# Kernel optimization log

Hardware: AMD Instinct MI355X
Metric: run time of the kernel (lower is better)

Reference implementation:

```python
import jax, jax.numpy as jnp
import numpy as np

TOP_K = 8
ALPHA = 0.1
EPS = 1e-20


def setup_inputs() -> dict:
    key = jax.random.key(0)
    k1, k2 = jax.random.split(key)
    B, S, D, E = 4, 8192, 1024, 64
    hidden_states = jax.random.normal(k1, (B, S, D), dtype=jnp.float32)
    # kaiming_uniform_(a=sqrt(5)) on [E, D] -> bound = 1/sqrt(D)
    bound = 1.0 / np.sqrt(D)
    W = jax.random.uniform(k2, (E, D), dtype=jnp.float32, minval=-bound, maxval=bound)
    return {"hidden_states": hidden_states, "W": W}


def reference(hidden_states, W):
    B, S, D = hidden_states.shape
    E = W.shape[0]
    x = hidden_states.reshape(-1, D)                       # [T, D], T = B*S
    logits = jnp.einsum('td,ed->te', x, W)                 # [T, E]
    scores = jax.nn.softmax(logits, axis=-1)               # [T, E]
    top_k_weights, top_k_idx = jax.lax.top_k(scores, TOP_K)  # [T, K]
    # norm_topk_experts renormalization
    top_k_weights = top_k_weights / (top_k_weights.sum(axis=-1, keepdims=True) + EPS)
    # seq_aux loss: per-batch expert selection counts via scatter-add
    idx = top_k_idx.reshape(B, -1)                         # [B, S*K]
    ce = jnp.zeros((B, E), dtype=jnp.float32).at[jnp.arange(B)[:, None], idx].add(1.0)
    mean_scores = scores.reshape(B, S, E).mean(axis=1)     # [B, E]
    aux_loss = (ce * mean_scores).sum(axis=1).mean() * ALPHA
    return top_k_idx, top_k_weights, aux_loss
```

## Files before the change

### kernel.cpp

```cpp
#include <hip/hip_runtime.h>

#define TOKS   32768
#define NEXP   64
#define DDIM   1024
#define SEQ    8192
#define NBATCH 4
#define TPB    64
#define STR    68
#define CSTR   21
#define BK     64
#define NCHK   (DDIM / BK)
#define WTILE  16384
#define XTILE  16384

typedef __attribute__((ext_vector_type(8)))  short short8v;
typedef __attribute__((ext_vector_type(16))) float f32x16;

__device__ __forceinline__ unsigned f2bf(float x) {
  unsigned u = __float_as_uint(x);
  return (u + 0x7fffu + ((u >> 16) & 1u)) >> 16;
}
__device__ __forceinline__ float bf2f(unsigned h) { return __uint_as_float(h << 16); }

__device__ __forceinline__ void gload_lds16(const void* g, void* s) {
  __builtin_amdgcn_global_load_lds(
      (const __attribute__((address_space(1))) unsigned int*)g,
      (__attribute__((address_space(3))) unsigned int*)s, 16, 0, 0);
}

__device__ __forceinline__ void conv8(const float4 p0, const float4 p1,
                                      unsigned* h, unsigned* lo) {
  float ff[8] = {p0.x, p0.y, p0.z, p0.w, p1.x, p1.y, p1.z, p1.w};
#pragma unroll
  for (int i = 0; i < 4; ++i) {
    unsigned h0 = f2bf(ff[2 * i]), h1 = f2bf(ff[2 * i + 1]);
    h[i] = h0 | (h1 << 16);
    unsigned l0 = f2bf(ff[2 * i] - bf2f(h0));
    unsigned l1 = f2bf(ff[2 * i + 1] - bf2f(h1));
    lo[i] = l0 | (l1 << 16);
  }
}

__global__ void moe_wsplit(const float* __restrict__ W, ushort* __restrict__ W2) {
  const int sid = blockIdx.x * 256 + threadIdx.x;
  const int p  = sid & 15;
  const int e  = (sid >> 4) & 63;
  const int kc = sid >> 10;
  const int sl = p ^ (e & 15);
  const int k0 = kc * BK + (sl & 7) * 8;
  const float* src = W + (size_t)e * DDIM + k0;
  float f[8];
  *(float4*)&f[0] = *(const float4*)src;
  *(float4*)&f[4] = *(const float4*)(src + 4);
  ushort o[8];
  if (sl < 8) {
#pragma unroll
    for (int j = 0; j < 8; ++j) o[j] = (ushort)f2bf(f[j]);
  } else {
#pragma unroll
    for (int j = 0; j < 8; ++j) {
      unsigned hb = f2bf(f[j]);
      o[j] = (ushort)f2bf(f[j] - bf2f(hb));
    }
  }
  *(short8v*)(W2 + (size_t)sid * 8) = *(const short8v*)o;
}

__global__ __launch_bounds__(256, 2) void moe_gate_main(
    const float* __restrict__ X, const ushort* __restrict__ W2,
    float* __restrict__ out, float* __restrict__ gsum, float* __restrict__ gce,
    int* __restrict__ flag_cnt, int* __restrict__ flag_tok)
{
  __shared__ __align__(16) char smem[65536];

  float* xs   = (float*)smem;
  float* wsm  = (float*)(smem + 17408);
  float* red  = (float*)(smem + 34816);
  float* gmx  = (float*)(smem + 35840);
  float* cval = (float*)(smem + 36096);
  int*   cidx = (int*)  (smem + 41472);
  int*   hist = (int*)  (smem + 46848);

  const int tid = threadIdx.x;
  const int tok_base = blockIdx.x * TPB;
  const int bb = blockIdx.x >> 7;

  const int l = tid & 63, q = tid >> 6;
  const int wm = q >> 1, wn = q & 1;
  const int rr = l & 31;
  const int kh = l >> 5;

  const char* Xb = (const char*)X + (size_t)tok_base * DDIM * 4;
  int gofs[4];
#pragma unroll
  for (int i = 0; i < 4; ++i) {
    const int r  = 16 * q + 4 * i + (l >> 4);
    const int sl = (l & 15) ^ (r & 15);
    gofs[i] = r * 4096 + sl * 16;
  }
  const char* w2c = (const char*)W2;

  const int arow = (wm * 32 + rr) * 256;
  const int brow = (wn * 32 + rr) * 256;
  const int rxor = rr & 15;

  f32x16 accA = (f32x16)0.0f, accB = (f32x16)0.0f;

#pragma unroll
  for (int i = 0; i < 4; ++i)
    gload_lds16(Xb + gofs[i], smem + q * 4096 + i * 1024);
#pragma unroll
  for (int i = 0; i < 4; ++i)
    gload_lds16(w2c + q * 4096 + i * 1024 + l * 16, smem + 32768 + q * 4096 + i * 1024);
  __syncthreads();

  int cur = 0;
#pragma unroll 1
  for (int kc = 0; kc < NCHK; ++kc) {
    if (kc + 1 < NCHK) {
      const char* xg = Xb + (kc + 1) * 256;
      char* xd = smem + (cur ^ 1) * XTILE + q * 4096;
#pragma unroll
      for (int i = 0; i < 4; ++i) gload_lds16(xg + gofs[i], xd + i * 1024);
      const char* wg = w2c + (size_t)(kc + 1) * WTILE + q * 4096 + l * 16;
      char* wd = smem + 32768 + (cur ^ 1) * WTILE + q * 4096;
#pragma unroll
      for (int i = 0; i < 4; ++i) gload_lds16(wg + i * 1024, wd + i * 1024);
    }
    const char* ta = smem + cur * XTILE + arow;
    const char* tb = smem + 32768 + cur * WTILE + brow;
#pragma unroll
    for (int s = 0; s < 4; ++s) {
      const int q0 = 4 * s + 2 * kh;
      float4 f0 = *(const float4*)(ta + ((q0 ^ rxor) * 16));
      float4 f1 = *(const float4*)(ta + (((q0 + 1) ^ rxor) * 16));
      unsigned ah[4], al[4];
      conv8(f0, f1, ah, al);
      short8v bh = *(const short8v*)(tb + (((2 * s + kh) ^ rxor) * 16));
      short8v bl = *(const short8v*)(tb + (((8 + 2 * s + kh) ^ rxor) * 16));
      union { short8v v; unsigned u[4]; } ua, ul;
#pragma unroll
      for (int i = 0; i < 4; ++i) { ua.u[i] = ah[i]; ul.u[i] = al[i]; }
      accA = __builtin_amdgcn_mfma_f32_32x32x16_bf16(ua.v, bh, accA, 0, 0, 0);
      accB = __builtin_amdgcn_mfma_f32_32x32x16_bf16(ul.v, bh, accB, 0, 0, 0);
      accA = __builtin_amdgcn_mfma_f32_32x32x16_bf16(ua.v, bl, accA, 0, 0, 0);
    }
    __syncthreads();
    cur ^= 1;
  }

  {
    const int ccol = wn * 32 + rr;
#pragma unroll
    for (int r = 0; r < 16; ++r) {
      const int trow = wm * 32 + (r & 3) + 8 * (r >> 2) + 4 * kh;
      wsm[trow * STR + ccol] = accA[r] + accB[r];
    }
  }
  if (tid < 64) hist[tid] = 0;
  __syncthreads();

  float* logits  = wsm;
  float* scoresT = xs;
  const int t = l;

  float m = -__builtin_huge_valf();
#pragma unroll
  for (int e = 0; e < 16; ++e) m = fmaxf(m, logits[t * STR + q * 16 + e]);
  red[q * 64 + t] = m;
  __syncthreads();
  float gm = fmaxf(fmaxf(red[t], red[64 + t]), fmaxf(red[128 + t], red[192 + t]));
  if (q == 0) gmx[t] = gm;
  float z = 0.0f;
#pragma unroll
  for (int e = 0; e < 16; ++e) {
    float ev = expf(logits[t * STR + q * 16 + e] - gm);
    scoresT[(q * 16 + e) * STR + t] = ev;
    z += ev;
  }
  __syncthreads();
  red[q * 64 + t] = z;
  __syncthreads();
  float Z = red[t] + red[64 + t] + red[128 + t] + red[192 + t];
  float invZ = 1.0f / Z;
#pragma unroll
  for (int e = 0; e < 16; ++e) scoresT[(q * 16 + e) * STR + t] *= invZ;
  __syncthreads();

  {
    const int e = l, g = q;
    float s = 0.0f;
#pragma unroll
    for (int tt = 0; tt < 16; ++tt) s += scoresT[e * STR + g * 16 + tt];
    red[g * 64 + e] = s;
  }
  __syncthreads();
  if (tid < 64) {
    float tot = red[tid] + red[64 + tid] + red[128 + tid] + red[192 + tid];
    atomicAdd(&gsum[bb * 64 + tid], tot);
  }

  if (tid < 128) {
    const int h = tid >> 6;
    const int eb = h * 32;
#pragma unroll 1
    for (int k = 0; k < 9; ++k) {
      float mv = -1.0f; int mi = eb;
#pragma unroll 4
      for (int e = 0; e < 32; ++e) {
        float v = scoresT[(eb + e) * STR + t];
        if (v > mv) { mv = v; mi = eb + e; }
      }
      cval[t * CSTR + h * 9 + k] = mv;
      cidx[t * CSTR + h * 9 + k] = mi;
      scoresT[mi * STR + t] = -1.0f;
    }
  }
  __syncthreads();

  if (tid < 64) {
    float wv[9]; int wi[8];
#pragma unroll 1
    for (int k = 0; k < 9; ++k) {
      float mv = -1.0f; int mj = 0;
#pragma unroll 3
      for (int j = 0; j < 18; ++j) {
        float v = cval[t * CSTR + j];
        if (v > mv) { mv = v; mj = j; }
      }
      wv[k] = mv;
      if (k < 8) {
        wi[k] = cidx[t * CSTR + mj];
        atomicAdd(&hist[wi[k]], 1);
      }
      cval[t * CSTR + mj] = -1.0f;
    }
    bool flag = false;
#pragma unroll
    for (int k = 0; k < 8; ++k)
      if (wv[k + 1] >= wv[k] * (1.0f - 2.0e-5f)) flag = true;
    if (flag) {
      int p = atomicAdd(flag_cnt, 1);
      flag_tok[p] = tok_base + t;
    }
    double ed[8]; double den = 0.0;
#pragma unroll
    for (int k = 0; k < 8; ++k) {
      ed[k] = exp((double)logits[t * STR + wi[k]] - (double)gmx[t]);
      den += ed[k];
    }
    const size_t tg = (size_t)(tok_base + t);
    *(float4*)(out + tg * 8) =
        make_float4((float)wi[0], (float)wi[1], (float)wi[2], (float)wi[3]);
    *(float4*)(out + tg * 8 + 4) =
        make_float4((float)wi[4], (float)wi[5], (float)wi[6], (float)wi[7]);
    *(float4*)(out + (size_t)TOKS * 8 + tg * 8) =
        make_float4((float)(ed[0] / den), (float)(ed[1] / den),
                    (float)(ed[2] / den), (float)(ed[3] / den));
    *(float4*)(out + (size_t)TOKS * 8 + tg * 8 + 4) =
        make_float4((float)(ed[4] / den), (float)(ed[5] / den),
                    (float)(ed[6] / den), (float)(ed[7] / den));
  }
  __syncthreads();
  if (tid < 64) atomicAdd(&gce[bb * 64 + tid], (float)hist[tid]);
}

__global__ __launch_bounds__(256) void moe_refine(
    const float* __restrict__ X, const float* __restrict__ W,
    float* __restrict__ out, float* __restrict__ gce,
    const int* __restrict__ flag_cnt, const int* __restrict__ flag_tok)
{
  __shared__ __align__(16) float xrow[DDIM];
  __shared__ double part[4][NEXP];
  const int tid = threadIdx.x;
  const int n = *flag_cnt;
  const int e = tid & 63;
  const int c = tid >> 6;
#pragma unroll 1
  for (int it = blockIdx.x; it < n; it += 256) {
    const int tok = flag_tok[it];
    __syncthreads();
    *(float4*)&xrow[tid * 4] = *(const float4*)&X[(size_t)tok * DDIM + tid * 4];
    __syncthreads();
    const float* wr = W + (size_t)e * DDIM + c * 256;
    const float* xr = xrow + c * 256;
    double s0 = 0.0, s1 = 0.0, s2 = 0.0, s3 = 0.0;
#pragma unroll 4
    for (int j = 0; j < 256; j += 4) {
      s0 += (double)xr[j]     * (double)wr[j];
      s1 += (double)xr[j + 1] * (double)wr[j + 1];
      s2 += (double)xr[j + 2] * (double)wr[j + 2];
      s3 += (double)xr[j + 3] * (double)wr[j + 3];
    }
    part[c][e] = (s0 + s1) + (s2 + s3);
    __syncthreads();
    if (tid < 64) {
      double cur = (part[0][e] + part[1][e]) + (part[2][e] + part[3][e]);
      int wi[8]; double wl[8];
#pragma unroll 1
      for (int k = 0; k < 8; ++k) {
        double mv = cur; int mi = e;
#pragma unroll
        for (int off = 1; off < 64; off <<= 1) {
          double ov = __shfl_xor(mv, off);
          int    oi = __shfl_xor(mi, off);
          if (ov > mv || (ov == mv && oi < mi)) { mv = ov; mi = oi; }
        }
        wi[k] = mi; wl[k] = mv;
        if (e == mi) cur = -1.0e300;
      }
      if (e == 0) {
        int olde[8];
#pragma unroll
        for (int k = 0; k < 8; ++k) olde[k] = (int)out[(size_t)tok * 8 + k];
        double ex[8]; double den = 0.0;
#pragma unroll
        for (int k = 0; k < 8; ++k) { ex[k] = exp(wl[k] - wl[0]); den += ex[k]; }
#pragma unroll
        for (int k = 0; k < 8; ++k) {
          out[(size_t)tok * 8 + k] = (float)wi[k];
          out[(size_t)TOKS * 8 + (size_t)tok * 8 + k] = (float)(ex[k] / den);
        }
        const int bbb = tok >> 13;
#pragma unroll 1
        for (int k = 0; k < 8; ++k) {
          bool in_new = false, in_old = false;
          for (int j = 0; j < 8; ++j) {
            if (wi[j] == olde[k]) in_new = true;
            if (olde[j] == wi[k]) in_old = true;
          }
          if (!in_new) atomicAdd(&gce[bbb * 64 + olde[k]], -1.0f);
          if (!in_old) atomicAdd(&gce[bbb * 64 + wi[k]], 1.0f);
        }
      }
    }
  }
}

__global__ void moe_gate_aux(const float* __restrict__ gsum,
                             const float* __restrict__ gce,
                             float* __restrict__ out)
{
  __shared__ float r[256];
  const int tid = threadIdx.x;
  r[tid] = gce[tid] * gsum[tid];
  __syncthreads();
  for (int s = 128; s > 0; s >>= 1) {
    if (tid < s) r[tid] += r[tid + s];
    __syncthreads();
  }
  if (tid == 0)
    out[(size_t)TOKS * 16] = 0.1f * r[0] / ((float)SEQ * (float)NBATCH);
}

extern "C" void kernel_launch(void* const* d_in, const int* in_sizes, int n_in,
                              void* d_out, int out_size, void* d_ws, size_t ws_size,
                              hipStream_t stream)
{
  const float* X = (const float*)d_in[0];
  const float* W = (const float*)d_in[1];
  float* out  = (float*)d_out;
  float* gsum = (float*)d_ws;
  float* gce  = gsum + NBATCH * NEXP;
  int* flag_cnt = (int*)((char*)d_ws + 2048);
  int* flag_tok = (int*)((char*)d_ws + 2176);
  ushort* W2 = (ushort*)((char*)d_ws + (1 << 20));

  hipMemsetAsync(d_ws, 0, 2176, stream);
  moe_wsplit<<<64, 256, 0, stream>>>(W, W2);
  moe_gate_main<<<TOKS / TPB, 256, 0, stream>>>(X, W2, out, gsum, gce, flag_cnt, flag_tok);
  moe_refine<<<256, 256, 0, stream>>>(X, W, out, gce, flag_cnt, flag_tok);
  moe_gate_aux<<<1, 256, 0, stream>>>(gsum, gce, out);
}
```

Before: 236.5 us.

## Deepen GEMM prefetch pipeline to four stages with half-size K chunks

Halves the K chunk from 64 to 32 and uses four LDS buffers in place of two, so three chunks are in flight while one is computed. Fixed __syncthreads are replaced with explicit vmcnt waits plus barriers, which lets later loads stay outstanding across the barrier. The W pre-split kernel and the swizzles are rewritten for the new chunk geometry. The intent is to hide global-load latency better, at the cost of twice as many barriers and loop iterations.

```diff
diff --git a/kernel.cpp b/kernel.cpp
--- a/kernel.cpp
+++ b/kernel.cpp
@@ -8,10 +8,11 @@
 #define TPB    64
 #define STR    68
 #define CSTR   21
-#define BK     64
+#define BK     32
 #define NCHK   (DDIM / BK)
-#define WTILE  16384
-#define XTILE  16384
+#define XT     8192
+#define WT     8192
+#define WBASE  32768
 
 typedef __attribute__((ext_vector_type(8)))  short short8v;
 typedef __attribute__((ext_vector_type(16))) float f32x16;
@@ -41,19 +42,32 @@
   }
 }
 
+#define WAITBAR8() do { \
+  asm volatile("s_waitcnt vmcnt(8) lgkmcnt(0)" ::: "memory"); \
+  __builtin_amdgcn_s_barrier(); \
+  __builtin_amdgcn_sched_barrier(0); } while (0)
+#define WAITBAR4() do { \
+  asm volatile("s_waitcnt vmcnt(4) lgkmcnt(0)" ::: "memory"); \
+  __builtin_amdgcn_s_barrier(); \
+  __builtin_amdgcn_sched_barrier(0); } while (0)
+#define WAITBAR0() do { \
+  asm volatile("s_waitcnt vmcnt(0) lgkmcnt(0)" ::: "memory"); \
+  __builtin_amdgcn_s_barrier(); \
+  __builtin_amdgcn_sched_barrier(0); } while (0)
+
 __global__ void moe_wsplit(const float* __restrict__ W, ushort* __restrict__ W2) {
   const int sid = blockIdx.x * 256 + threadIdx.x;
-  const int p  = sid & 15;
-  const int e  = (sid >> 4) & 63;
-  const int kc = sid >> 10;
-  const int sl = p ^ (e & 15);
-  const int k0 = kc * BK + (sl & 7) * 8;
+  const int p  = sid & 7;
+  const int e  = (sid >> 3) & 63;
+  const int kc = sid >> 9;
+  const int sl = p ^ (e & 7);
+  const int k0 = kc * BK + (sl & 3) * 8;
   const float* src = W + (size_t)e * DDIM + k0;
   float f[8];
   *(float4*)&f[0] = *(const float4*)src;
   *(float4*)&f[4] = *(const float4*)(src + 4);
   ushort o[8];
-  if (sl < 8) {
+  if (sl < 4) {
 #pragma unroll
     for (int j = 0; j < 8; ++j) o[j] = (ushort)f2bf(f[j]);
   } else {
@@ -91,63 +105,68 @@
   const int kh = l >> 5;
 
   const char* Xb = (const char*)X + (size_t)tok_base * DDIM * 4;
-  int gofs[4];
-#pragma unroll
-  for (int i = 0; i < 4; ++i) {
-    const int r  = 16 * q + 4 * i + (l >> 4);
-    const int sl = (l & 15) ^ (r & 15);
-    gofs[i] = r * 4096 + sl * 16;
+  int gofs[2];
+#pragma unroll
+  for (int i = 0; i < 2; ++i) {
+    const int r  = 16 * q + 8 * i + (l >> 3);
+    const int p  = l & 7;
+    gofs[i] = r * 4096 + (((p ^ (r & 7)) << 4));
   }
   const char* w2c = (const char*)W2;
-
-  const int arow = (wm * 32 + rr) * 256;
-  const int brow = (wn * 32 + rr) * 256;
-  const int rxor = rr & 15;
+  const int sofs = q * 2048 + l * 16;
+
+  const int arow = (wm * 32 + rr) * 128;
+  const int brow = (wn * 32 + rr) * 128;
+  const int rxor = rr & 7;
 
   f32x16 accA = (f32x16)0.0f, accB = (f32x16)0.0f;
 
-#pragma unroll
-  for (int i = 0; i < 4; ++i)
-    gload_lds16(Xb + gofs[i], smem + q * 4096 + i * 1024);
-#pragma unroll
-  for (int i = 0; i < 4; ++i)
-    gload_lds16(w2c + q * 4096 + i * 1024 + l * 16, smem + 32768 + q * 4096 + i * 1024);
-  __syncthreads();
-
-  int cur = 0;
-#pragma unroll 1
-  for (int kc = 0; kc < NCHK; ++kc) {
-    if (kc + 1 < NCHK) {
-      const char* xg = Xb + (kc + 1) * 256;
-      char* xd = smem + (cur ^ 1) * XTILE + q * 4096;
-#pragma unroll
-      for (int i = 0; i < 4; ++i) gload_lds16(xg + gofs[i], xd + i * 1024);
-      const char* wg = w2c + (size_t)(kc + 1) * WTILE + q * 4096 + l * 16;
-      char* wd = smem + 32768 + (cur ^ 1) * WTILE + q * 4096;
-#pragma unroll
-      for (int i = 0; i < 4; ++i) gload_lds16(wg + i * 1024, wd + i * 1024);
-    }
-    const char* ta = smem + cur * XTILE + arow;
-    const char* tb = smem + 32768 + cur * WTILE + brow;
-#pragma unroll
-    for (int s = 0; s < 4; ++s) {
-      const int q0 = 4 * s + 2 * kh;
-      float4 f0 = *(const float4*)(ta + ((q0 ^ rxor) * 16));
-      float4 f1 = *(const float4*)(ta + (((q0 + 1) ^ rxor) * 16));
-      unsigned ah[4], al[4];
-      conv8(f0, f1, ah, al);
-      short8v bh = *(const short8v*)(tb + (((2 * s + kh) ^ rxor) * 16));
-      short8v bl = *(const short8v*)(tb + (((8 + 2 * s + kh) ^ rxor) * 16));
-      union { short8v v; unsigned u[4]; } ua, ul;
-#pragma unroll
-      for (int i = 0; i < 4; ++i) { ua.u[i] = ah[i]; ul.u[i] = al[i]; }
-      accA = __builtin_amdgcn_mfma_f32_32x32x16_bf16(ua.v, bh, accA, 0, 0, 0);
-      accB = __builtin_amdgcn_mfma_f32_32x32x16_bf16(ul.v, bh, accB, 0, 0, 0);
-      accA = __builtin_amdgcn_mfma_f32_32x32x16_bf16(ua.v, bl, accA, 0, 0, 0);
-    }
-    __syncthreads();
-    cur ^= 1;
-  }
+#define STAGE(n) do { \
+    char* xd = smem + ((n) & 3) * XT + q * 2048; \
+    const char* xg = Xb + (n) * 128; \
+    gload_lds16(xg + gofs[0], xd); \
+    gload_lds16(xg + gofs[1], xd + 1024); \
+    char* wd = smem + WBASE + ((n) & 3) * WT + q * 2048; \
+    const char* wg = w2c + (size_t)(n) * WT + sofs; \
+    gload_lds16(wg, wd); \
+    gload_lds16(wg + 1024, wd + 1024); } while (0)
+
+#define COMPUTE(kc) do { \
+    const char* ta = smem + ((kc) & 3) * XT + arow; \
+    const char* tb = smem + WBASE + ((kc) & 3) * WT + brow; \
+    _Pragma("unroll") \
+    for (int s = 0; s < 2; ++s) { \
+      const int q0 = 4 * s + 2 * kh; \
+      float4 f0 = *(const float4*)(ta + ((q0 ^ rxor) << 4)); \
+      float4 f1 = *(const float4*)(ta + (((q0 + 1) ^ rxor) << 4)); \
+      unsigned ah[4], al[4]; \
+      conv8(f0, f1, ah, al); \
+      short8v bh = *(const short8v*)(tb + (((2 * s + kh) ^ rxor) << 4)); \
+      short8v bl = *(const short8v*)(tb + (((4 + 2 * s + kh) ^ rxor) << 4)); \
+      union { short8v v; unsigned u[4]; } ua, ul; \
+      _Pragma("unroll") \
+      for (int i = 0; i < 4; ++i) { ua.u[i] = ah[i]; ul.u[i] = al[i]; } \
+      accA = __builtin_amdgcn_mfma_f32_32x32x16_bf16(ua.v, bh, accA, 0, 0, 0); \
+      accB = __builtin_amdgcn_mfma_f32_32x32x16_bf16(ul.v, bh, accB, 0, 0, 0); \
+      accA = __builtin_amdgcn_mfma_f32_32x32x16_bf16(ua.v, bl, accA, 0, 0, 0); \
+    } } while (0)
+
+  STAGE(0); STAGE(1); STAGE(2);
+  WAITBAR8();
+
+#pragma unroll 1
+  for (int kc = 0; kc < NCHK - 3; ++kc) {
+    STAGE(kc + 3);
+    COMPUTE(kc);
+    WAITBAR8();
+  }
+  COMPUTE(29); WAITBAR4();
+  COMPUTE(30); WAITBAR0();
+  COMPUTE(31);
+  __syncthreads();
+
+#undef STAGE
+#undef COMPUTE
 
   {
     const int ccol = wn * 32 + rr;
```

New measurement: 245.7 us. +3.9%, slower.
